# Kernel optimization log

Hardware: AMD Instinct MI355X
Metric: run time of the kernel (lower is better)

Reference implementation:

```python
import jax, jax.numpy as jnp
import numpy as np

B, S, N, F = 4, 256, 128, 64
D = 128          # d_model == 2*F so encoder/decoder dims agree
NH = 4           # hard-coded num_heads in both MHA blocks


def _linear(x, w, b):
    # torch nn.Linear: y = x @ W.T + b, W: (out, in)
    return x @ w.T + b


def _mha(q, k, v, w_in, b_in, w_out, b_out, nh):
    # torch nn.MultiheadAttention (batch_first=True) with packed in_proj
    bq, sq, e = q.shape
    hd = e // nh
    qp = _linear(q, w_in[:e], b_in[:e])
    kp = _linear(k, w_in[e:2 * e], b_in[e:2 * e])
    vp = _linear(v, w_in[2 * e:], b_in[2 * e:])
    qh = qp.reshape(bq, sq, nh, hd)
    kh = kp.reshape(bq, k.shape[1], nh, hd)
    vh = vp.reshape(bq, v.shape[1], nh, hd)
    scores = jnp.einsum('bqhd,bkhd->bhqk', qh, kh) / np.sqrt(hd).astype(np.float32)
    attn = jax.nn.softmax(scores, axis=-1)
    out = jnp.einsum('bhqk,bkhd->bqhd', attn, vh).reshape(bq, sq, e)
    return _linear(out, w_out, b_out)


def _pos_enc(s, d):
    pos = jnp.arange(s, dtype=jnp.float32)[:, None]
    div = jnp.exp(jnp.arange(0, d, 2, dtype=jnp.float32) * (-np.log(10000.0) / d))
    pe = jnp.zeros((s, d), dtype=jnp.float32)
    pe = pe.at[:, 0::2].set(jnp.sin(pos * div))
    pe = pe.at[:, 1::2].set(jnp.cos(pos * div))
    return pe


def _haar_decouple(x):
    # exact vectorized pywt haar dwt + single-branch idwt (even seq_len)
    b, s, n, f = x.shape
    pairs = x.reshape(b, s // 2, 2, n, f)
    avg = (pairs[:, :, 0] + pairs[:, :, 1]) * 0.5  # idwt(cA, None) value
    dif = (pairs[:, :, 0] - pairs[:, :, 1]) * 0.5  # idwt(None, cD) value
    x_l = jnp.stack([avg, avg], axis=2).reshape(b, s, n, f)
    x_h = jnp.stack([dif, -dif], axis=2).reshape(b, s, n, f)
    return x_l, x_h


def setup_inputs() -> dict:
    key = jax.random.key(0)
    ks = jax.random.split(key, 32)
    p = lambda i, shp: jax.random.normal(ks[i], shp, jnp.float32) * 0.02
    return {
        'x': jax.random.normal(ks[0], (B, S, N, F), jnp.float32),
        'ts': jax.random.randint(ks[1], (B, S), 0, 252),
        'ta_w_in': p(2, (3 * D, D)), 'ta_b_in': p(3, (3 * D,)),
        'ta_w_out': p(4, (D, D)), 'ta_b_out': p(5, (D,)),
        'conv_w': p(6, (D, 2 * F, 3)), 'conv_b': p(7, (D,)),
        'pl_w': p(8, (D, D)), 'pl_b': p(9, (D,)),
        'ph_w': p(10, (D, D)), 'ph_b': p(11, (D,)),
        'as_w_in': p(12, (3 * D, D)), 'as_b_in': p(13, (3 * D,)),
        'as_w_out': p(14, (D, D)), 'as_b_out': p(15, (D,)),
        'ac_w_in': p(16, (3 * D, D)), 'ac_b_in': p(17, (3 * D,)),
        'ac_w_out': p(18, (D, D)), 'ac_b_out': p(19, (D,)),
        'rl_w': p(20, (1, D)), 'rl_b': p(21, (1,)),
        'cl_w': p(22, (2, D)), 'cl_b': p(23, (2,)),
        'rf_w': p(24, (1, D)), 'rf_b': p(25, (1,)),
        'cf_w': p(26, (2, D)), 'cf_b': p(27, (2,)),
    }


def reference(x, ts, ta_w_in, ta_b_in, ta_w_out, ta_b_out, conv_w, conv_b,
              pl_w, pl_b, ph_w, ph_b, as_w_in, as_b_in, as_w_out, as_b_out,
              ac_w_in, ac_b_in, ac_w_out, ac_b_out, rl_w, rl_b, cl_w, cl_b,
              rf_w, rf_b, cf_w, cf_b):
    b, s, n, f = x.shape
    # --- DecouplingFlowLayer (vectorized haar) ---
    x_l, x_h = _haar_decouple(x)
    xl_cat = jnp.concatenate([x, x_l], axis=-1)  # (b,s,n,2f)
    xh_cat = jnp.concatenate([x, x_h], axis=-1)
    e = 2 * f
    # --- DualFrequencyEncoder ---
    pe = _pos_enc(s, e)
    xl_flat = xl_cat.transpose(0, 2, 1, 3).reshape(b * n, s, e) + pe
    x_tatt = _mha(xl_flat, xl_flat, xl_flat, ta_w_in, ta_b_in, ta_w_out, ta_b_out, NH)
    x_l_gat = x_tatt.reshape(b, s, n, e)  # faithful raw .view() as in torch
    xh_flat = xh_cat.transpose(0, 2, 3, 1).reshape(b * n, e, s)
    conv = jax.lax.conv_general_dilated(
        xh_flat, conv_w, window_strides=(1,), padding=[(2, 2)],
        rhs_dilation=(2,), dimension_numbers=('NCH', 'OIH', 'NCH'))
    conv = jax.nn.relu(conv + conv_b[None, :, None])
    x_h_gat = conv.reshape(b, n, -1, s).transpose(0, 3, 1, 2)  # (b,s,n,D)
    d = x_h_gat.shape[-1]
    # ts -> time_embedding is computed then discarded in the original forward: dead code
    # --- DualFrequencyFusionDecoder ---
    y_l = x_l_gat.reshape(b * n, s, d)
    y_h = x_h_gat.reshape(b * n, s, d)
    q_l = _linear(y_l, pl_w, pl_b)
    k_h = _linear(y_h, ph_w, ph_b)
    y_l2 = _linear(q_l, pl_w, pl_b)  # predictor_l applied twice, as in torch
    lreg = _linear(y_l2, rl_w, rl_b).reshape(b, s, n)
    lcla = jax.nn.softmax(_linear(y_l2, cl_w, cl_b), axis=-1).reshape(b, s, n, 2)
    a_self = _mha(q_l, q_l, q_l, as_w_in, as_b_in, as_w_out, as_b_out, NH)
    a_cross = _mha(q_l, k_h, k_h, ac_w_in, ac_b_in, ac_w_out, ac_b_out, NH)
    fused = (a_self + a_cross).reshape(b, s, n, d)
    reg = _linear(fused, rf_w, rf_b)[..., 0]
    cla = jax.nn.softmax(_linear(fused, cf_w, cf_b), axis=-1)
    return reg, cla, lreg, lcla
```

## Files before the change

### kernel.cpp

```cpp
#include <hip/hip_runtime.h>
#include <hip/hip_bf16.h>

typedef __attribute__((ext_vector_type(8))) short short8v;
typedef __attribute__((ext_vector_type(4))) short short4v;
typedef __attribute__((ext_vector_type(4))) float f32x4;
typedef __hip_bfloat16 bh;

constexpr long SF_ELEMS = 131072L * 128;
#define MFMA16(a, b, c) __builtin_amdgcn_mfma_f32_16x16x32_bf16((a), (b), (c), 0, 0, 0)

__device__ __forceinline__ short bh_bits(float x) {
  bh h = __float2bfloat16(x);
  return *reinterpret_cast<short*>(&h);
}


__global__ __launch_bounds__(256) void sf_wcvt(const float* __restrict__ s0, const float* __restrict__ s1,
                                               const float* __restrict__ s2, const float* __restrict__ s3,
                                               const float* __restrict__ s4, const float* __restrict__ s5,
                                               const float* __restrict__ s6, const float* __restrict__ s7,
                                               const float* __restrict__ cw,
                                               bh* __restrict__ dst) {
  int i = blockIdx.x * 256 + threadIdx.x;
  float v;
  if      (i <  49152) v = s0[i];
  else if (i <  65536) v = s1[i - 49152];
  else if (i <  81920) v = s2[i - 65536];
  else if (i <  98304) v = s3[i - 81920];
  else if (i < 147456) v = s4[i - 98304];
  else if (i < 163840) v = s5[i - 147456];
  else if (i < 212992) v = s6[i - 163840];
  else if (i < 229376) v = s7[i - 212992];
  else if (i < 278528) {
    int j = i - 229376;
    int tap = j >> 14, rem = j & 16383;
    v = cw[rem * 3 + tap];
  } else return;
  dst[i] = __float2bfloat16(v);
}

__global__ __launch_bounds__(256) void sf_pe(float* __restrict__ pe) {
  int i = blockIdx.x * 256 + threadIdx.x;
  int e = i & 127, s = i >> 7;
  int ii = e >> 1;
  float dv = expf(-0.0719557945041855f * (float)(2 * ii));
  float ang = (float)s * dv;
  pe[i] = (e & 1) ? cosf(ang) : sinf(ang);
}

__global__ __launch_bounds__(256) void sf_buildzx(const float* __restrict__ x,
                                                  const float* __restrict__ pe,
                                                  bh* __restrict__ z,
                                                  bh* __restrict__ xh) {
  long i = (long)blockIdx.x * 256 + threadIdx.x;
  if (i >= SF_ELEMS) return;
  int e = (int)(i & 127);
  int s = (int)((i >> 7) & 255);
  int r = (int)(i >> 15);
  int b = r >> 7, stk = r & 127;
  float zv, hv;
  if (e < 64) {
    float val = x[(((long)b * 256 + s) * 128 + stk) * 64 + e];
    zv = val; hv = val;
  } else {
    int f = e - 64;
    int t2 = s >> 1;
    float a0 = x[(((long)b * 256 + 2 * t2) * 128 + stk) * 64 + f];
    float a1 = x[(((long)b * 256 + 2 * t2 + 1) * 128 + stk) * 64 + f];
    zv = 0.5f * (a0 + a1);
    float d = 0.5f * (a0 - a1);
    hv = (s & 1) ? -d : d;
  }
  z[i] = __float2bfloat16(zv + pe[s * 128 + e]);
  xh[i] = __float2bfloat16(hv);
}

__global__ __launch_bounds__(256) void sf_attnp(const bh* Qsrc, const bh* KVsrc,
                                                const bh* __restrict__ Win,
                                                const float* __restrict__ bin,
                                                bh* __restrict__ O) {
  __shared__ bh Ks[256][36];
  __shared__ bh Vt[32][260];
  __shared__ bh QP[4][64][36];
  const int t = threadIdx.x, lane = t & 63, w = t >> 6;
  const int lr = lane & 15, lg = lane >> 4;
  const int bn = blockIdx.x >> 2, h = blockIdx.x & 3;
  const long R0 = (long)bn * 256;
  const int ch = h * 32;
  const f32x4 z4 = {0.f, 0.f, 0.f, 0.f};
  const float SC2 = 0.2550351f;
  {
    short8v wq[2][4];
#pragma unroll
    for (int n = 0; n < 2; ++n)
#pragma unroll
      for (int ks = 0; ks < 4; ++ks)
        wq[n][ks] = *reinterpret_cast<const short8v*>(Win + (long)(ch + n * 16 + lr) * 128 + ks * 32 + lg * 8);
#pragma unroll
    for (int m2 = 0; m2 < 4; ++m2) {
      short8v asv[4];
#pragma unroll
      for (int ks = 0; ks < 4; ++ks)
        asv[ks] = *reinterpret_cast<const short8v*>(Qsrc + (R0 + w * 64 + m2 * 16 + lr) * 128 + ks * 32 + lg * 8);
#pragma unroll
      for (int n = 0; n < 2; ++n) {
        f32x4 acc = z4;
#pragma unroll
        for (int ks = 0; ks < 4; ++ks) acc = MFMA16(asv[ks], wq[n][ks], acc);
        float bb = bin[ch + n * 16 + lr];
#pragma unroll
        for (int r = 0; r < 4; ++r)
          QP[w][m2 * 16 + 4 * lg + r][n * 16 + lr] = __float2bfloat16((acc[r] + bb) * SC2);
      }
    }
  }
  {
    short8v wk[2][4], wv[2][4];
#pragma unroll
    for (int n = 0; n < 2; ++n)
#pragma unroll
      for (int ks = 0; ks < 4; ++ks) {
        wk[n][ks] = *reinterpret_cast<const short8v*>(Win + (long)(128 + ch + n * 16 + lr) * 128 + ks * 32 + lg * 8);
        wv[n][ks] = *reinterpret_cast<const short8v*>(Win + (long)(256 + ch + n * 16 + lr) * 128 + ks * 32 + lg * 8);
      }
#pragma unroll
    for (int m2 = 0; m2 < 4; ++m2) {
      short8v asv[4];
#pragma unroll
      for (int ks = 0; ks < 4; ++ks)
        asv[ks] = *reinterpret_cast<const short8v*>(KVsrc + (R0 + w * 64 + m2 * 16 + lr) * 128 + ks * 32 + lg * 8);
#pragma unroll
      for (int n = 0; n < 2; ++n) {
        f32x4 ak = z4, av = z4;
#pragma unroll
        for (int ks = 0; ks < 4; ++ks) {
          ak = MFMA16(asv[ks], wk[n][ks], ak);
          av = MFMA16(asv[ks], wv[n][ks], av);
        }
        float bk = bin[128 + ch + n * 16 + lr];
        float bv = bin[256 + ch + n * 16 + lr];
#pragma unroll
        for (int r = 0; r < 4; ++r)
          Ks[w * 64 + m2 * 16 + 4 * lg + r][n * 16 + lr] = __float2bfloat16(ak[r] + bk);
        short4v pv;
#pragma unroll
        for (int r = 0; r < 4; ++r) pv[r] = bh_bits(av[r] + bv);
        *reinterpret_cast<short4v*>(&Vt[n * 16 + lr][w * 64 + m2 * 16 + 4 * lg]) = pv;
      }
    }
  }
  __syncthreads();
  short8v aq[4];
#pragma unroll
  for (int mt = 0; mt < 4; ++mt)
    aq[mt] = *reinterpret_cast<const short8v*>(&QP[w][mt * 16 + lr][lg * 8]);
  bh* plp = &QP[w][0][0];
  f32x4 Oacc[4][2];
  float psum[4] = {0.f, 0.f, 0.f, 0.f};
#pragma unroll
  for (int mt = 0; mt < 4; ++mt) { Oacc[mt][0] = z4; Oacc[mt][1] = z4; }
#pragma unroll
  for (int kt = 0; kt < 4; ++kt) {
    short8v bvf[2][2];
#pragma unroll
    for (int dt = 0; dt < 2; ++dt)
#pragma unroll
      for (int ks = 0; ks < 2; ++ks)
        bvf[dt][ks] = *reinterpret_cast<const short8v*>(&Vt[dt * 16 + lr][kt * 64 + ks * 32 + lg * 8]);
#pragma unroll
    for (int mt = 0; mt < 4; ++mt) {
      f32x4 st[4];
#pragma unroll
      for (int nt = 0; nt < 4; ++nt) {
        short8v bk = *reinterpret_cast<const short8v*>(&Ks[kt * 64 + nt * 16 + lr][lg * 8]);
        st[nt] = MFMA16(bk, aq[mt], z4);
      }
      float ps = 0.f;
#pragma unroll
      for (int nt = 0; nt < 4; ++nt) {
        float p0 = exp2f(st[nt][0]);
        float p1 = exp2f(st[nt][1]);
        float p2 = exp2f(st[nt][2]);
        float p3 = exp2f(st[nt][3]);
        ps += (p0 + p1) + (p2 + p3);
        short4v pk;
        pk[0] = bh_bits(p0); pk[1] = bh_bits(p1); pk[2] = bh_bits(p2); pk[3] = bh_bits(p3);
        *reinterpret_cast<short4v*>(&plp[lr * 72 + nt * 16 + 4 * lg]) = pk;
      }
      psum[mt] += ps;
#pragma unroll
      for (int ks = 0; ks < 2; ++ks) {
        short8v ap = *reinterpret_cast<const short8v*>(&plp[lr * 72 + ks * 32 + lg * 8]);
        Oacc[mt][0] = MFMA16(ap, bvf[0][ks], Oacc[mt][0]);
        Oacc[mt][1] = MFMA16(ap, bvf[1][ks], Oacc[mt][1]);
      }
    }
  }
#pragma unroll
  for (int mt = 0; mt < 4; ++mt) {
    float ps = psum[mt];
    ps += __shfl_xor(ps, 16, 64);
    ps += __shfl_xor(ps, 32, 64);
    float inv = 1.f / ps;
#pragma unroll
    for (int r = 0; r < 4; ++r) {
      float invr = __shfl(inv, 4 * lg + r, 64);
      long row = R0 + w * 64 + mt * 16 + 4 * lg + r;
      O[row * 128 + ch + lr]      = __float2bfloat16(Oacc[mt][0][r] * invr);
      O[row * 128 + ch + 16 + lr] = __float2bfloat16(Oacc[mt][1][r] * invr);
    }
  }
}

__global__ __launch_bounds__(256) void sf_convkh(const bh* __restrict__ Xh,
                                                 const bh* __restrict__ Wr,
                                                 const float* __restrict__ cbias,
                                                 const bh* __restrict__ Wph,
                                                 const float* __restrict__ bph,
                                                 bh* __restrict__ KH) {
  __shared__ bh Lw[4][32][140];
  const int t = threadIdx.x, lane = t & 63, w = t >> 6;
  const int lr = lane & 15, lg = lane >> 4;
  const int bnc = blockIdx.x >> 1;
  const int half = blockIdx.x & 1;
  const int b = bnc >> 7, stk = bnc & 127;
  const int R0 = half * 128 + w * 32;
  const f32x4 z4 = {0.f, 0.f, 0.f, 0.f};
  const short8v zf = {0, 0, 0, 0, 0, 0, 0, 0};
  f32x4 acc[2][8];
#pragma unroll
  for (int m = 0; m < 2; ++m)
#pragma unroll
    for (int n = 0; n < 8; ++n) acc[m][n] = z4;
#pragma unroll
  for (int tap = 0; tap < 3; ++tap) {
    const int shift = 2 * tap - 2;
#pragma unroll
    for (int ks = 0; ks < 4; ++ks) {
      int s0 = R0 + lr + shift;
      int s1 = s0 + 16;
      short8v a0 = zf, a1 = zf;
      if ((unsigned)s0 < 256u)
        a0 = *reinterpret_cast<const short8v*>(Xh + ((long)bnc * 256 + s0) * 128 + ks * 32 + lg * 8);
      if ((unsigned)s1 < 256u)
        a1 = *reinterpret_cast<const short8v*>(Xh + ((long)bnc * 256 + s1) * 128 + ks * 32 + lg * 8);
#pragma unroll
      for (int n = 0; n < 8; ++n) {
        short8v bb = *reinterpret_cast<const short8v*>(Wr + (long)tap * 16384 + (long)(n * 16 + lr) * 128 + ks * 32 + lg * 8);
        acc[0][n] = MFMA16(a0, bb, acc[0][n]);
        acc[1][n] = MFMA16(a1, bb, acc[1][n]);
      }
    }
  }
#pragma unroll
  for (int n = 0; n < 8; ++n) {
    float bv = cbias[n * 16 + lr];
#pragma unroll
    for (int m = 0; m < 2; ++m)
#pragma unroll
      for (int r = 0; r < 4; ++r)
        Lw[w][m * 16 + 4 * lg + r][n * 16 + lr] = __float2bfloat16(fmaxf(acc[m][n][r] + bv, 0.f));
  }
  {
    short8v a2[2][4];
#pragma unroll
    for (int ks = 0; ks < 4; ++ks) {
      a2[0][ks] = *reinterpret_cast<const short8v*>(&Lw[w][lr][ks * 32 + lg * 8]);
      a2[1][ks] = *reinterpret_cast<const short8v*>(&Lw[w][16 + lr][ks * 32 + lg * 8]);
    }
    f32x4 ac2[2][8];
#pragma unroll
    for (int m = 0; m < 2; ++m)
#pragma unroll
      for (int n = 0; n < 8; ++n) ac2[m][n] = z4;
#pragma unroll
    for (int ks = 0; ks < 4; ++ks)
#pragma unroll
      for (int n = 0; n < 8; ++n) {
        short8v b2 = *reinterpret_cast<const short8v*>(Wph + (long)(n * 16 + lr) * 128 + ks * 32 + lg * 8);
        ac2[0][n] = MFMA16(a2[0][ks], b2, ac2[0][n]);
        ac2[1][n] = MFMA16(a2[1][ks], b2, ac2[1][n]);
      }
#pragma unroll
    for (int n = 0; n < 8; ++n) {
      float bv = bph[n * 16 + lr];
#pragma unroll
      for (int m = 0; m < 2; ++m)
#pragma unroll
        for (int r = 0; r < 4; ++r)
          Lw[w][m * 16 + 4 * lg + r][n * 16 + lr] = __float2bfloat16(ac2[m][n][r] + bv);
    }
  }
#pragma unroll
  for (int c = 0; c < 8; ++c) {
    int row_l = c * 4 + lg;
    int sc = R0 + row_l;
    int rp = b * 128 + (sc >> 1);
    int sp = ((sc & 1) << 7) + stk;
    short8v v = *reinterpret_cast<const short8v*>(&Lw[w][row_l][lr * 8]);
    *reinterpret_cast<short8v*>(KH + ((long)rp * 256 + sp) * 128 + lr * 8) = v;
  }
}

__global__ __launch_bounds__(256) void sf_encdec(const bh* __restrict__ X,
                                                 const bh* __restrict__ Wo, const float* __restrict__ bo,
                                                 const bh* __restrict__ Wpl, const float* __restrict__ bpl,
                                                 const float* __restrict__ rw, const float* __restrict__ rb,
                                                 const float* __restrict__ cw, const float* __restrict__ cb,
                                                 bh* __restrict__ Yq, float* __restrict__ out,
                                                 long off_reg, long off_cla) {
  __shared__ bh Lw[4][32][140];
  __shared__ float hw[3][128];
  const int t = threadIdx.x, lane = t & 63, w = t >> 6;
  const int lr = lane & 15, lg = lane >> 4;
  const long R0 = (long)blockIdx.x * 128 + w * 32;
  const f32x4 z4 = {0.f, 0.f, 0.f, 0.f};
  if (t < 128) { hw[0][t] = rw[t]; hw[1][t] = cw[t]; hw[2][t] = cw[128 + t]; }
  {
    short8v a[2][4];
#pragma unroll
    for (int ks = 0; ks < 4; ++ks) {
      a[0][ks] = *reinterpret_cast<const short8v*>(X + (R0 + lr) * 128 + ks * 32 + lg * 8);
      a[1][ks] = *reinterpret_cast<const short8v*>(X + (R0 + 16 + lr) * 128 + ks * 32 + lg * 8);
    }
    f32x4 acc[2][8];
#pragma unroll
    for (int m = 0; m < 2; ++m)
#pragma unroll
      for (int n = 0; n < 8; ++n) acc[m][n] = z4;
#pragma unroll
    for (int ks = 0; ks < 4; ++ks)
#pragma unroll
      for (int n = 0; n < 8; ++n) {
        short8v b = *reinterpret_cast<const short8v*>(Wo + (long)(n * 16 + lr) * 128 + ks * 32 + lg * 8);
        acc[0][n] = MFMA16(a[0][ks], b, acc[0][n]);
        acc[1][n] = MFMA16(a[1][ks], b, acc[1][n]);
      }
#pragma unroll
    for (int n = 0; n < 8; ++n) {
      float bv = bo[n * 16 + lr];
#pragma unroll
      for (int m = 0; m < 2; ++m)
#pragma unroll
        for (int r = 0; r < 4; ++r)
          Lw[w][m * 16 + 4 * lg + r][n * 16 + lr] = __float2bfloat16(acc[m][n][r] + bv);
    }
  }
#pragma unroll
  for (int stage = 0; stage < 2; ++stage) {
    short8v a[2][4];
#pragma unroll
    for (int ks = 0; ks < 4; ++ks) {
      a[0][ks] = *reinterpret_cast<const short8v*>(&Lw[w][lr][ks * 32 + lg * 8]);
      a[1][ks] = *reinterpret_cast<const short8v*>(&Lw[w][16 + lr][ks * 32 + lg * 8]);
    }
    f32x4 acc[2][8];
#pragma unroll
    for (int m = 0; m < 2; ++m)
#pragma unroll
      for (int n = 0; n < 8; ++n) acc[m][n] = z4;
#pragma unroll
    for (int ks = 0; ks < 4; ++ks)
#pragma unroll
      for (int n = 0; n < 8; ++n) {
        short8v b = *reinterpret_cast<const short8v*>(Wpl + (long)(n * 16 + lr) * 128 + ks * 32 + lg * 8);
        acc[0][n] = MFMA16(a[0][ks], b, acc[0][n]);
        acc[1][n] = MFMA16(a[1][ks], b, acc[1][n]);
      }
#pragma unroll
    for (int n = 0; n < 8; ++n) {
      float bv = bpl[n * 16 + lr];
#pragma unroll
      for (int m = 0; m < 2; ++m)
#pragma unroll
        for (int r = 0; r < 4; ++r)
          Lw[w][m * 16 + 4 * lg + r][n * 16 + lr] = __float2bfloat16(acc[m][n][r] + bv);
    }
    if (stage == 0) {
#pragma unroll
      for (int c = 0; c < 8; ++c) {
        int row_l = c * 4 + lg;
        short8v v = *reinterpret_cast<const short8v*>(&Lw[w][row_l][lr * 8]);
        *reinterpret_cast<short8v*>(Yq + (R0 + row_l) * 128 + lr * 8) = v;
      }
    }
  }
  __syncthreads();
  {
    const int rr = lane >> 1, hh = lane & 1;
    float d0 = 0.f, d1 = 0.f, d2 = 0.f;
#pragma unroll
    for (int j = 0; j < 8; ++j) {
      short8v v8 = *reinterpret_cast<const short8v*>(&Lw[w][rr][hh * 64 + j * 8]);
      const bh* vv = reinterpret_cast<const bh*>(&v8);
#pragma unroll
      for (int k = 0; k < 8; ++k) {
        float f = __bfloat162float(vv[k]);
        int c = hh * 64 + j * 8 + k;
        d0 = fmaf(f, hw[0][c], d0);
        d1 = fmaf(f, hw[1][c], d1);
        d2 = fmaf(f, hw[2][c], d2);
      }
    }
    d0 += __shfl_xor(d0, 1, 64);
    d1 += __shfl_xor(d1, 1, 64);
    d2 += __shfl_xor(d2, 1, 64);
    if (hh == 0) {
      long row = R0 + rr;
      d0 += rb[0]; d1 += cb[0]; d2 += cb[1];
      float mx = fmaxf(d1, d2);
      float e1 = __expf(d1 - mx), e2 = __expf(d2 - mx);
      float inv = 1.f / (e1 + e2);
      out[off_reg + row] = d0;
      out[off_cla + row * 2] = e1 * inv;
      out[off_cla + row * 2 + 1] = e2 * inv;
    }
  }
}

__global__ __launch_bounds__(256) void sf_fin2(const bh* __restrict__ Xs,
                                               const bh* __restrict__ Was, const float* __restrict__ bs,
                                               const bh* __restrict__ Xc,
                                               const bh* __restrict__ Wac, const float* __restrict__ bc,
                                               const float* __restrict__ rw, const float* __restrict__ rb,
                                               const float* __restrict__ cw, const float* __restrict__ cb,
                                               float* __restrict__ out, long off_reg, long off_cla) {
  __shared__ bh Lw[4][32][140];
  __shared__ float hw[3][128];
  const int t = threadIdx.x, lane = t & 63, w = t >> 6;
  const int lr = lane & 15, lg = lane >> 4;
  const long R0 = (long)blockIdx.x * 128 + w * 32;
  const f32x4 z4 = {0.f, 0.f, 0.f, 0.f};
  if (t < 128) { hw[0][t] = rw[t]; hw[1][t] = cw[t]; hw[2][t] = cw[128 + t]; }
  {
    f32x4 acc[2][8];
#pragma unroll
    for (int m = 0; m < 2; ++m)
#pragma unroll
      for (int n = 0; n < 8; ++n) acc[m][n] = z4;
    {
      short8v a[2][4];
#pragma unroll
      for (int ks = 0; ks < 4; ++ks) {
        a[0][ks] = *reinterpret_cast<const short8v*>(Xs + (R0 + lr) * 128 + ks * 32 + lg * 8);
        a[1][ks] = *reinterpret_cast<const short8v*>(Xs + (R0 + 16 + lr) * 128 + ks * 32 + lg * 8);
      }
#pragma unroll
      for (int ks = 0; ks < 4; ++ks)
#pragma unroll
        for (int n = 0; n < 8; ++n) {
          short8v b = *reinterpret_cast<const short8v*>(Was + (long)(n * 16 + lr) * 128 + ks * 32 + lg * 8);
          acc[0][n] = MFMA16(a[0][ks], b, acc[0][n]);
          acc[1][n] = MFMA16(a[1][ks], b, acc[1][n]);
        }
    }
    {
      short8v a[2][4];
#pragma unroll
      for (int ks = 0; ks < 4; ++ks) {
        a[0][ks] = *reinterpret_cast<const short8v*>(Xc + (R0 + lr) * 128 + ks * 32 + lg * 8);
        a[1][ks] = *reinterpret_cast<const short8v*>(Xc + (R0 + 16 + lr) * 128 + ks * 32 + lg * 8);
      }
#pragma unroll
      for (int ks = 0; ks < 4; ++ks)
#pragma unroll
        for (int n = 0; n < 8; ++n) {
          short8v b = *reinterpret_cast<const short8v*>(Wac + (long)(n * 16 + lr) * 128 + ks * 32 + lg * 8);
          acc[0][n] = MFMA16(a[0][ks], b, acc[0][n]);
          acc[1][n] = MFMA16(a[1][ks], b, acc[1][n]);
        }
    }
#pragma unroll
    for (int n = 0; n < 8; ++n) {
      float bv = bs[n * 16 + lr] + bc[n * 16 + lr];
#pragma unroll
      for (int m = 0; m < 2; ++m)
#pragma unroll
        for (int r = 0; r < 4; ++r)
          Lw[w][m * 16 + 4 * lg + r][n * 16 + lr] = __float2bfloat16(acc[m][n][r] + bv);
    }
  }
  __syncthreads();
  {
    const int rr = lane >> 1, hh = lane & 1;
    float d0 = 0.f, d1 = 0.f, d2 = 0.f;
#pragma unroll
    for (int j = 0; j < 8; ++j) {
      short8v v8 = *reinterpret_cast<const short8v*>(&Lw[w][rr][hh * 64 + j * 8]);
      const bh* vv = reinterpret_cast<const bh*>(&v8);
#pragma unroll
      for (int k = 0; k < 8; ++k) {
        float f = __bfloat162float(vv[k]);
        int c = hh * 64 + j * 8 + k;
        d0 = fmaf(f, hw[0][c], d0);
        d1 = fmaf(f, hw[1][c], d1);
        d2 = fmaf(f, hw[2][c], d2);
      }
    }
    d0 += __shfl_xor(d0, 1, 64);
    d1 += __shfl_xor(d1, 1, 64);
    d2 += __shfl_xor(d2, 1, 64);
    if (hh == 0) {
      long row = R0 + rr;
      d0 += rb[0]; d1 += cb[0]; d2 += cb[1];
      float mx = fmaxf(d1, d2);
      float e1 = __expf(d1 - mx), e2 = __expf(d2 - mx);
      float inv = 1.f / (e1 + e2);
      out[off_reg + row] = d0;
      out[off_cla + row * 2] = e1 * inv;
      out[off_cla + row * 2 + 1] = e2 * inv;
    }
  }
}

extern "C" void kernel_launch(void* const* d_in, const int* in_sizes, int n_in,
                              void* d_out, int out_size, void* d_ws, size_t ws_size,
                              hipStream_t stream) {
  (void)in_sizes; (void)n_in; (void)out_size; (void)ws_size;
  const float* x       = (const float*)d_in[0];
  const float* ta_w_in = (const float*)d_in[2];
  const float* ta_b_in = (const float*)d_in[3];
  const float* ta_w_o  = (const float*)d_in[4];
  const float* ta_b_o  = (const float*)d_in[5];
  const float* conv_w  = (const float*)d_in[6];
  const float* conv_b  = (const float*)d_in[7];
  const float* pl_w    = (const float*)d_in[8];
  const float* pl_b    = (const float*)d_in[9];
  const float* ph_w    = (const float*)d_in[10];
  const float* ph_b    = (const float*)d_in[11];
  const float* as_w_in = (const float*)d_in[12];
  const float* as_b_in = (const float*)d_in[13];
  const float* as_w_o  = (const float*)d_in[14];
  const float* as_b_o  = (const float*)d_in[15];
  const float* ac_w_in = (const float*)d_in[16];
  const float* ac_b_in = (const float*)d_in[17];
  const float* ac_w_o  = (const float*)d_in[18];
  const float* ac_b_o  = (const float*)d_in[19];
  const float* rl_w    = (const float*)d_in[20];
  const float* rl_b    = (const float*)d_in[21];
  const float* cl_w    = (const float*)d_in[22];
  const float* cl_b    = (const float*)d_in[23];
  const float* rf_w    = (const float*)d_in[24];
  const float* rf_b    = (const float*)d_in[25];
  const float* cf_w    = (const float*)d_in[26];
  const float* cf_b    = (const float*)d_in[27];
  float* out = (float*)d_out;

  bh* S0 = (bh*)d_ws;
  bh* S1 = S0 + SF_ELEMS;
  bh* S2 = S1 + SF_ELEMS;
  bh* S3 = S2 + SF_ELEMS;
  bh* S4 = S3 + SF_ELEMS;
  bh* A  = S4 + SF_ELEMS;
  float* PE = (float*)(A + 278528);

  dim3 blk(256);
  const int GZ = (int)(SF_ELEMS / 256);
  const int GL = 1024;

  sf_wcvt<<<1088, blk, 0, stream>>>(ta_w_in, ta_w_o, pl_w, ph_w, ac_w_in, ac_w_o,
                                    as_w_in, as_w_o, conv_w, A);
  sf_pe<<<128, blk, 0, stream>>>(PE);

  sf_buildzx<<<GZ, blk, 0, stream>>>(x, PE, S0, S3);
  sf_attnp<<<2048, blk, 0, stream>>>(S0, S0, A, ta_b_in, S1);
  sf_encdec<<<GL, blk, 0, stream>>>(S1, A + 49152, ta_b_o, A + 65536, pl_b,
                                    rl_w, rl_b, cl_w, cl_b, S2, out,
                                    393216L, 524288L);
  sf_convkh<<<1024, blk, 0, stream>>>(S3, A + 229376, conv_b, A + 81920, ph_b, S0);

  sf_attnp<<<2048, blk, 0, stream>>>(S2, S0, A + 98304, ac_b_in, S3);

  sf_attnp<<<2048, blk, 0, stream>>>(S2, S2, A + 163840, as_b_in, S1);

  sf_fin2<<<GL, blk, 0, stream>>>(S1, A + 212992, as_b_o, S3, A + 147456, ac_b_o,
                                  rf_w, rf_b, cf_w, cf_b, out, 0L, 131072L);
}
```

Before: 455.7 us.

## Pad high-frequency buffer with zero guard rows and split conv kernel finer

The high-frequency tensor is now written into a padded layout of 260 rows per series, and a new small kernel zeroes the two guard rows on each side. This lets the dilated conv load all three tap fragments unconditionally, without bounds checks. The conv+projection kernel now handles 16 rows per wave instead of 32 and launches twice as many blocks, which raises parallelism and lowers register use. In exchange, each weight fragment is reused across half as many rows, so weight loads per output double, and there is one extra launch. The padded buffer extends past its nominal slot into the next workspace region.

```diff
diff --git a/kernel.cpp b/kernel.cpp
--- a/kernel.cpp
+++ b/kernel.cpp
@@ -48,10 +48,19 @@
   pe[i] = (e & 1) ? cosf(ang) : sinf(ang);
 }
 
+__global__ __launch_bounds__(256) void sf_zguard(bh* __restrict__ xhp) {
+  int i = blockIdx.x * 256 + threadIdx.x;
+  int bnc = i >> 9;
+  int j = i & 511;
+  int q = j >> 7;
+  int row = (q < 2) ? q : 256 + q;
+  xhp[((long)bnc * 260 + row) * 128 + (j & 127)] = __float2bfloat16(0.f);
+}
+
 __global__ __launch_bounds__(256) void sf_buildzx(const float* __restrict__ x,
                                                   const float* __restrict__ pe,
                                                   bh* __restrict__ z,
-                                                  bh* __restrict__ xh) {
+                                                  bh* __restrict__ xhp) {
   long i = (long)blockIdx.x * 256 + threadIdx.x;
   if (i >= SF_ELEMS) return;
   int e = (int)(i & 127);
@@ -72,7 +81,7 @@
     hv = (s & 1) ? -d : d;
   }
   z[i] = __float2bfloat16(zv + pe[s * 128 + e]);
-  xh[i] = __float2bfloat16(hv);
+  xhp[((long)r * 260 + s + 2) * 128 + e] = __float2bfloat16(hv);
 }
 
 __global__ __launch_bounds__(256) void sf_attnp(const bh* Qsrc, const bh* KVsrc,
@@ -212,87 +221,73 @@
   }
 }
 
-__global__ __launch_bounds__(256) void sf_convkh(const bh* __restrict__ Xh,
+__global__ __launch_bounds__(256) void sf_convkh(const bh* __restrict__ Xhp,
                                                  const bh* __restrict__ Wr,
                                                  const float* __restrict__ cbias,
                                                  const bh* __restrict__ Wph,
                                                  const float* __restrict__ bph,
                                                  bh* __restrict__ KH) {
-  __shared__ bh Lw[4][32][140];
+  __shared__ bh Lw[4][16][140];
   const int t = threadIdx.x, lane = t & 63, w = t >> 6;
   const int lr = lane & 15, lg = lane >> 4;
-  const int bnc = blockIdx.x >> 1;
-  const int half = blockIdx.x & 1;
+  const int bnc = blockIdx.x >> 2;
+  const int quarter = blockIdx.x & 3;
   const int b = bnc >> 7, stk = bnc & 127;
-  const int R0 = half * 128 + w * 32;
+  const int R0 = quarter * 64 + w * 16;
   const f32x4 z4 = {0.f, 0.f, 0.f, 0.f};
-  const short8v zf = {0, 0, 0, 0, 0, 0, 0, 0};
-  f32x4 acc[2][8];
-#pragma unroll
-  for (int m = 0; m < 2; ++m)
-#pragma unroll
-    for (int n = 0; n < 8; ++n) acc[m][n] = z4;
-#pragma unroll
-  for (int tap = 0; tap < 3; ++tap) {
-    const int shift = 2 * tap - 2;
-#pragma unroll
-    for (int ks = 0; ks < 4; ++ks) {
-      int s0 = R0 + lr + shift;
-      int s1 = s0 + 16;
-      short8v a0 = zf, a1 = zf;
-      if ((unsigned)s0 < 256u)
-        a0 = *reinterpret_cast<const short8v*>(Xh + ((long)bnc * 256 + s0) * 128 + ks * 32 + lg * 8);
-      if ((unsigned)s1 < 256u)
-        a1 = *reinterpret_cast<const short8v*>(Xh + ((long)bnc * 256 + s1) * 128 + ks * 32 + lg * 8);
+  short8v a[3][4];
+#pragma unroll
+  for (int tap = 0; tap < 3; ++tap)
+#pragma unroll
+    for (int ks = 0; ks < 4; ++ks)
+      a[tap][ks] = *reinterpret_cast<const short8v*>(
+          Xhp + ((long)bnc * 260 + R0 + lr + 2 * tap) * 128 + ks * 32 + lg * 8);
+  f32x4 acc[8];
+#pragma unroll
+  for (int n = 0; n < 8; ++n) acc[n] = z4;
+#pragma unroll
+  for (int ks = 0; ks < 4; ++ks)
+#pragma unroll
+    for (int tap = 0; tap < 3; ++tap)
 #pragma unroll
       for (int n = 0; n < 8; ++n) {
-        short8v bb = *reinterpret_cast<const short8v*>(Wr + (long)tap * 16384 + (long)(n * 16 + lr) * 128 + ks * 32 + lg * 8);
-        acc[0][n] = MFMA16(a0, bb, acc[0][n]);
-        acc[1][n] = MFMA16(a1, bb, acc[1][n]);
-      }
-    }
-  }
+        short8v bb = *reinterpret_cast<const short8v*>(
+            Wr + (long)tap * 16384 + (long)(n * 16 + lr) * 128 + ks * 32 + lg * 8);
+        acc[n] = MFMA16(a[tap][ks], bb, acc[n]);
+      }
 #pragma unroll
   for (int n = 0; n < 8; ++n) {
     float bv = cbias[n * 16 + lr];
 #pragma unroll
-    for (int m = 0; m < 2; ++m)
-#pragma unroll
-      for (int r = 0; r < 4; ++r)
-        Lw[w][m * 16 + 4 * lg + r][n * 16 + lr] = __float2bfloat16(fmaxf(acc[m][n][r] + bv, 0.f));
-  }
-  {
-    short8v a2[2][4];
-#pragma unroll
-    for (int ks = 0; ks < 4; ++ks) {
-      a2[0][ks] = *reinterpret_cast<const short8v*>(&Lw[w][lr][ks * 32 + lg * 8]);
-      a2[1][ks] = *reinterpret_cast<const short8v*>(&Lw[w][16 + lr][ks * 32 + lg * 8]);
-    }
-    f32x4 ac2[2][8];
-#pragma unroll
-    for (int m = 0; m < 2; ++m)
-#pragma unroll
-      for (int n = 0; n < 8; ++n) ac2[m][n] = z4;
+    for (int r = 0; r < 4; ++r)
+      Lw[w][4 * lg + r][n * 16 + lr] = __float2bfloat16(fmaxf(acc[n][r] + bv, 0.f));
+  }
+  {
+    short8v a2[4];
 #pragma unroll
     for (int ks = 0; ks < 4; ++ks)
+      a2[ks] = *reinterpret_cast<const short8v*>(&Lw[w][lr][ks * 32 + lg * 8]);
+    f32x4 ac2[8];
+#pragma unroll
+    for (int n = 0; n < 8; ++n) ac2[n] = z4;
+#pragma unroll
+    for (int ks = 0; ks < 4; ++ks)
 #pragma unroll
       for (int n = 0; n < 8; ++n) {
-        short8v b2 = *reinterpret_cast<const short8v*>(Wph + (long)(n * 16 + lr) * 128 + ks * 32 + lg * 8);
-        ac2[0][n] = MFMA16(a2[0][ks], b2, ac2[0][n]);
-        ac2[1][n] = MFMA16(a2[1][ks], b2, ac2[1][n]);
+        short8v b2 = *reinterpret_cast<const short8v*>(
+            Wph + (long)(n * 16 + lr) * 128 + ks * 32 + lg * 8);
+        ac2[n] = MFMA16(a2[ks], b2, ac2[n]);
       }
 #pragma unroll
     for (int n = 0; n < 8; ++n) {
       float bv = bph[n * 16 + lr];
 #pragma unroll
-      for (int m = 0; m < 2; ++m)
-#pragma unroll
-        for (int r = 0; r < 4; ++r)
-          Lw[w][m * 16 + 4 * lg + r][n * 16 + lr] = __float2bfloat16(ac2[m][n][r] + bv);
-    }
-  }
-#pragma unroll
-  for (int c = 0; c < 8; ++c) {
+      for (int r = 0; r < 4; ++r)
+        Lw[w][4 * lg + r][n * 16 + lr] = __float2bfloat16(ac2[n][r] + bv);
+    }
+  }
+#pragma unroll
+  for (int c = 0; c < 4; ++c) {
     int row_l = c * 4 + lg;
     int sc = R0 + row_l;
     int rp = b * 128 + (sc >> 1);
@@ -561,13 +556,14 @@
   sf_wcvt<<<1088, blk, 0, stream>>>(ta_w_in, ta_w_o, pl_w, ph_w, ac_w_in, ac_w_o,
                                     as_w_in, as_w_o, conv_w, A);
   sf_pe<<<128, blk, 0, stream>>>(PE);
+  sf_zguard<<<1024, blk, 0, stream>>>(S3);
 
   sf_buildzx<<<GZ, blk, 0, stream>>>(x, PE, S0, S3);
   sf_attnp<<<2048, blk, 0, stream>>>(S0, S0, A, ta_b_in, S1);
   sf_encdec<<<GL, blk, 0, stream>>>(S1, A + 49152, ta_b_o, A + 65536, pl_b,
                                     rl_w, rl_b, cl_w, cl_b, S2, out,
                                     393216L, 524288L);
-  sf_convkh<<<1024, blk, 0, stream>>>(S3, A + 229376, conv_b, A + 81920, ph_b, S0);
+  sf_convkh<<<2048, blk, 0, stream>>>(S3, A + 229376, conv_b, A + 81920, ph_b, S0);
 
   sf_attnp<<<2048, blk, 0, stream>>>(S2, S0, A + 98304, ac_b_in, S3);
 
```

After: 502.2 us. 1.1x slower.

## Fold predictor linear layers into attention in-projection weights algebraically

Applied to the files above, without the earlier changes.

Precomputes composed weight matrices (W_in·W_pl, W_in·W_ph, W_pl·W_pl) and folded biases in small setup kernels. Attention projections then consume the pre-predictor activations directly, so the conv kernel no longer applies the ph projection and encdec skips one of its two back-to-back pl GEMMs. This removes per-row GEMM work and the intermediate writes that went with it. In exchange, composing the weights in bf16 changes rounding and adds a few tiny launches.

```diff
diff --git a/kernel.cpp b/kernel.cpp
--- a/kernel.cpp
+++ b/kernel.cpp
@@ -35,6 +35,12 @@
     int j = i - 229376;
     int tap = j >> 14, rem = j & 16383;
     v = cw[rem * 3 + tap];
+  } else if (i < 294912) {
+    int j = i - 278528;
+    v = s2[(j & 127) * 128 + (j >> 7)];
+  } else if (i < 311296) {
+    int j = i - 294912;
+    v = s3[(j & 127) * 128 + (j >> 7)];
   } else return;
   dst[i] = __float2bfloat16(v);
 }
@@ -46,6 +52,72 @@
   float dv = expf(-0.0719557945041855f * (float)(2 * ii));
   float ang = (float)s * dv;
   pe[i] = (e & 1) ? cosf(ang) : sinf(ang);
+}
+
+__global__ __launch_bounds__(256) void sf_foldw(const bh* __restrict__ A0) {
+  __shared__ bh Lw[4][32][140];
+  const int t = threadIdx.x, lane = t & 63, w = t >> 6;
+  const int lr = lane & 15, lg = lane >> 4;
+  const f32x4 z4 = {0.f, 0.f, 0.f, 0.f};
+  const bh* Xp; const bh* Bp; bh* Op;
+  int blk = blockIdx.x;
+  bh* A = const_cast<bh*>(A0);
+  if (blk < 3)      { Xp = A0 + 163840 + blk * 16384; Bp = A0 + 278528; Op = A + 311296 + blk * 16384; }
+  else if (blk == 3){ Xp = A0 + 98304;                Bp = A0 + 278528; Op = A + 360448; }
+  else if (blk == 4){ Xp = A0 + 98304 + 16384;        Bp = A0 + 294912; Op = A + 376832; }
+  else if (blk == 5){ Xp = A0 + 98304 + 32768;        Bp = A0 + 294912; Op = A + 393216; }
+  else              { Xp = A0 + 65536;                Bp = A0 + 278528; Op = A + 409600; }
+  const long R0 = (long)w * 32;
+  short8v a[2][4];
+#pragma unroll
+  for (int ks = 0; ks < 4; ++ks) {
+    a[0][ks] = *reinterpret_cast<const short8v*>(Xp + (R0 + lr) * 128 + ks * 32 + lg * 8);
+    a[1][ks] = *reinterpret_cast<const short8v*>(Xp + (R0 + 16 + lr) * 128 + ks * 32 + lg * 8);
+  }
+  f32x4 acc[2][8];
+#pragma unroll
+  for (int m = 0; m < 2; ++m)
+#pragma unroll
+    for (int n = 0; n < 8; ++n) acc[m][n] = z4;
+#pragma unroll
+  for (int ks = 0; ks < 4; ++ks)
+#pragma unroll
+    for (int n = 0; n < 8; ++n) {
+      short8v b = *reinterpret_cast<const short8v*>(Bp + (long)(n * 16 + lr) * 128 + ks * 32 + lg * 8);
+      acc[0][n] = MFMA16(a[0][ks], b, acc[0][n]);
+      acc[1][n] = MFMA16(a[1][ks], b, acc[1][n]);
+    }
+#pragma unroll
+  for (int n = 0; n < 8; ++n)
+#pragma unroll
+    for (int m = 0; m < 2; ++m)
+#pragma unroll
+      for (int r = 0; r < 4; ++r)
+        Lw[w][m * 16 + 4 * lg + r][n * 16 + lr] = __float2bfloat16(acc[m][n][r]);
+#pragma unroll
+  for (int c = 0; c < 8; ++c) {
+    int row_l = c * 4 + lg;
+    short8v v = *reinterpret_cast<const short8v*>(&Lw[w][row_l][lr * 8]);
+    *reinterpret_cast<short8v*>(Op + (R0 + row_l) * 128 + lr * 8) = v;
+  }
+}
+
+__global__ __launch_bounds__(256) void sf_foldb(const float* __restrict__ as_w, const float* __restrict__ as_b,
+                                                const float* __restrict__ ac_w, const float* __restrict__ ac_b,
+                                                const float* __restrict__ pl_w, const float* __restrict__ pl_b,
+                                                const float* __restrict__ ph_b,
+                                                float* __restrict__ FB) {
+  int i = blockIdx.x * 256 + threadIdx.x;
+  if (i >= 896) return;
+  const float* w1; const float* b2; float b1;
+  if (i < 384)      { w1 = as_w + (long)i * 128;           b2 = pl_b; b1 = as_b[i]; }
+  else if (i < 512) { w1 = ac_w + (long)(i - 384) * 128;   b2 = pl_b; b1 = ac_b[i - 384]; }
+  else if (i < 640) { w1 = ac_w + (long)(i - 512 + 128) * 128; b2 = ph_b; b1 = ac_b[i - 512 + 128]; }
+  else if (i < 768) { w1 = ac_w + (long)(i - 640 + 256) * 128; b2 = ph_b; b1 = ac_b[i - 640 + 256]; }
+  else              { w1 = pl_w + (long)(i - 768) * 128;   b2 = pl_b; b1 = pl_b[i - 768]; }
+  float d = b1;
+  for (int k = 0; k < 128; ++k) d = fmaf(w1[k], b2[k], d);
+  FB[i] = d;
 }
 
 __global__ __launch_bounds__(256) void sf_buildzx(const float* __restrict__ x,
@@ -212,12 +284,10 @@
   }
 }
 
-__global__ __launch_bounds__(256) void sf_convkh(const bh* __restrict__ Xh,
-                                                 const bh* __restrict__ Wr,
-                                                 const float* __restrict__ cbias,
-                                                 const bh* __restrict__ Wph,
-                                                 const float* __restrict__ bph,
-                                                 bh* __restrict__ KH) {
+__global__ __launch_bounds__(256) void sf_convy(const bh* __restrict__ Xh,
+                                                const bh* __restrict__ Wr,
+                                                const float* __restrict__ cbias,
+                                                bh* __restrict__ Yh) {
   __shared__ bh Lw[4][32][140];
   const int t = threadIdx.x, lane = t & 63, w = t >> 6;
   const int lr = lane & 15, lg = lane >> 4;
@@ -261,36 +331,6 @@
       for (int r = 0; r < 4; ++r)
         Lw[w][m * 16 + 4 * lg + r][n * 16 + lr] = __float2bfloat16(fmaxf(acc[m][n][r] + bv, 0.f));
   }
-  {
-    short8v a2[2][4];
-#pragma unroll
-    for (int ks = 0; ks < 4; ++ks) {
-      a2[0][ks] = *reinterpret_cast<const short8v*>(&Lw[w][lr][ks * 32 + lg * 8]);
-      a2[1][ks] = *reinterpret_cast<const short8v*>(&Lw[w][16 + lr][ks * 32 + lg * 8]);
-    }
-    f32x4 ac2[2][8];
-#pragma unroll
-    for (int m = 0; m < 2; ++m)
-#pragma unroll
-      for (int n = 0; n < 8; ++n) ac2[m][n] = z4;
-#pragma unroll
-    for (int ks = 0; ks < 4; ++ks)
-#pragma unroll
-      for (int n = 0; n < 8; ++n) {
-        short8v b2 = *reinterpret_cast<const short8v*>(Wph + (long)(n * 16 + lr) * 128 + ks * 32 + lg * 8);
-        ac2[0][n] = MFMA16(a2[0][ks], b2, ac2[0][n]);
-        ac2[1][n] = MFMA16(a2[1][ks], b2, ac2[1][n]);
-      }
-#pragma unroll
-    for (int n = 0; n < 8; ++n) {
-      float bv = bph[n * 16 + lr];
-#pragma unroll
-      for (int m = 0; m < 2; ++m)
-#pragma unroll
-        for (int r = 0; r < 4; ++r)
-          Lw[w][m * 16 + 4 * lg + r][n * 16 + lr] = __float2bfloat16(ac2[m][n][r] + bv);
-    }
-  }
 #pragma unroll
   for (int c = 0; c < 8; ++c) {
     int row_l = c * 4 + lg;
@@ -298,16 +338,16 @@
     int rp = b * 128 + (sc >> 1);
     int sp = ((sc & 1) << 7) + stk;
     short8v v = *reinterpret_cast<const short8v*>(&Lw[w][row_l][lr * 8]);
-    *reinterpret_cast<short8v*>(KH + ((long)rp * 256 + sp) * 128 + lr * 8) = v;
+    *reinterpret_cast<short8v*>(Yh + ((long)rp * 256 + sp) * 128 + lr * 8) = v;
   }
 }
 
 __global__ __launch_bounds__(256) void sf_encdec(const bh* __restrict__ X,
                                                  const bh* __restrict__ Wo, const float* __restrict__ bo,
-                                                 const bh* __restrict__ Wpl, const float* __restrict__ bpl,
+                                                 const bh* __restrict__ Wpl2, const float* __restrict__ bpl2,
                                                  const float* __restrict__ rw, const float* __restrict__ rb,
                                                  const float* __restrict__ cw, const float* __restrict__ cb,
-                                                 bh* __restrict__ Yq, float* __restrict__ out,
+                                                 bh* __restrict__ Yl, float* __restrict__ out,
                                                  long off_reg, long off_cla) {
   __shared__ bh Lw[4][32][140];
   __shared__ float hw[3][128];
@@ -345,9 +385,14 @@
         for (int r = 0; r < 4; ++r)
           Lw[w][m * 16 + 4 * lg + r][n * 16 + lr] = __float2bfloat16(acc[m][n][r] + bv);
     }
-  }
-#pragma unroll
-  for (int stage = 0; stage < 2; ++stage) {
+#pragma unroll
+    for (int c = 0; c < 8; ++c) {
+      int row_l = c * 4 + lg;
+      short8v v = *reinterpret_cast<const short8v*>(&Lw[w][row_l][lr * 8]);
+      *reinterpret_cast<short8v*>(Yl + (R0 + row_l) * 128 + lr * 8) = v;
+    }
+  }
+  {
     short8v a[2][4];
 #pragma unroll
     for (int ks = 0; ks < 4; ++ks) {
@@ -363,26 +408,18 @@
     for (int ks = 0; ks < 4; ++ks)
 #pragma unroll
       for (int n = 0; n < 8; ++n) {
-        short8v b = *reinterpret_cast<const short8v*>(Wpl + (long)(n * 16 + lr) * 128 + ks * 32 + lg * 8);
+        short8v b = *reinterpret_cast<const short8v*>(Wpl2 + (long)(n * 16 + lr) * 128 + ks * 32 + lg * 8);
         acc[0][n] = MFMA16(a[0][ks], b, acc[0][n]);
         acc[1][n] = MFMA16(a[1][ks], b, acc[1][n]);
       }
 #pragma unroll
     for (int n = 0; n < 8; ++n) {
-      float bv = bpl[n * 16 + lr];
+      float bv = bpl2[n * 16 + lr];
 #pragma unroll
       for (int m = 0; m < 2; ++m)
 #pragma unroll
         for (int r = 0; r < 4; ++r)
           Lw[w][m * 16 + 4 * lg + r][n * 16 + lr] = __float2bfloat16(acc[m][n][r] + bv);
-    }
-    if (stage == 0) {
-#pragma unroll
-      for (int c = 0; c < 8; ++c) {
-        int row_l = c * 4 + lg;
-        short8v v = *reinterpret_cast<const short8v*>(&Lw[w][row_l][lr * 8]);
-        *reinterpret_cast<short8v*>(Yq + (R0 + row_l) * 128 + lr * 8) = v;
-      }
     }
   }
   __syncthreads();
@@ -552,26 +589,30 @@
   bh* S3 = S2 + SF_ELEMS;
   bh* S4 = S3 + SF_ELEMS;
   bh* A  = S4 + SF_ELEMS;
-  float* PE = (float*)(A + 278528);
+  float* PE = (float*)(A + 425984);
+  float* FB = PE + 32768;
 
   dim3 blk(256);
   const int GZ = (int)(SF_ELEMS / 256);
   const int GL = 1024;
 
-  sf_wcvt<<<1088, blk, 0, stream>>>(ta_w_in, ta_w_o, pl_w, ph_w, ac_w_in, ac_w_o,
+  sf_wcvt<<<1216, blk, 0, stream>>>(ta_w_in, ta_w_o, pl_w, ph_w, ac_w_in, ac_w_o,
                                     as_w_in, as_w_o, conv_w, A);
   sf_pe<<<128, blk, 0, stream>>>(PE);
+  sf_foldb<<<4, blk, 0, stream>>>(as_w_in, as_b_in, ac_w_in, ac_b_in,
+                                  pl_w, pl_b, ph_b, FB);
+  sf_foldw<<<7, blk, 0, stream>>>(A);
 
   sf_buildzx<<<GZ, blk, 0, stream>>>(x, PE, S0, S3);
   sf_attnp<<<2048, blk, 0, stream>>>(S0, S0, A, ta_b_in, S1);
-  sf_encdec<<<GL, blk, 0, stream>>>(S1, A + 49152, ta_b_o, A + 65536, pl_b,
+  sf_encdec<<<GL, blk, 0, stream>>>(S1, A + 49152, ta_b_o, A + 409600, FB + 768,
                                     rl_w, rl_b, cl_w, cl_b, S2, out,
                                     393216L, 524288L);
-  sf_convkh<<<1024, blk, 0, stream>>>(S3, A + 229376, conv_b, A + 81920, ph_b, S0);
-
-  sf_attnp<<<2048, blk, 0, stream>>>(S2, S0, A + 98304, ac_b_in, S3);
-
-  sf_attnp<<<2048, blk, 0, stream>>>(S2, S2, A + 163840, as_b_in, S1);
+  sf_convy<<<1024, blk, 0, stream>>>(S3, A + 229376, conv_b, S4);
+
+  sf_attnp<<<2048, blk, 0, stream>>>(S2, S4, A + 360448, FB + 384, S3);
+
+  sf_attnp<<<2048, blk, 0, stream>>>(S2, S2, A + 311296, FB, S1);
 
   sf_fin2<<<GL, blk, 0, stream>>>(S1, A + 212992, as_b_o, S3, A + 147456, ac_b_o,
                                   rf_w, rf_b, cf_w, cf_b, out, 0L, 131072L);
```

New measurement: 451.7 us, median of 3. No clear change (-0.9%).
